# Kernel tuning notes

Hardware: AMD Instinct MI355X
Metric: run time of the kernel (lower is better)

## Reference

```python
import jax, jax.numpy as jnp
import numpy as np

B, T, D_MODEL, HEAD_DIM = 16, 4096, 512, 64


def setup_inputs() -> dict:
    key = jax.random.key(0)
    kx, kq, kk, kv = jax.random.split(key, 4)
    x = jax.random.normal(kx, (B, T, D_MODEL), dtype=jnp.float32)
    # torch nn.Linear weights, stored pre-transposed as [in, out] for x @ W
    s = 1.0 / np.sqrt(D_MODEL)
    Wq = jax.random.uniform(kq, (D_MODEL, HEAD_DIM), jnp.float32, -s, s)
    Wk = jax.random.uniform(kk, (D_MODEL, HEAD_DIM), jnp.float32, -s, s)
    Wv = jax.random.uniform(kv, (D_MODEL, HEAD_DIM), jnp.float32, -s, s)
    return {"x": x, "Wq": Wq, "Wk": Wk, "Wv": Wv}


def reference(x, Wq, Wk, Wv):
    # Single-head causal self-attention (dropout in eval mode = identity)
    q = x @ Wq  # [B, T, h]
    k = x @ Wk
    v = x @ Wv
    scale = 1.0 / np.sqrt(HEAD_DIM).astype(np.float32)
    scores = jnp.einsum("bth,bsh->bts", q, k) * scale  # [B, T, T]
    t = scores.shape[1]
    causal = jnp.tril(jnp.ones((t, t), dtype=bool))
    scores = jnp.where(causal, scores, -jnp.inf)
    weights = jax.nn.softmax(scores, axis=-1)
    return jnp.einsum("bts,bsh->bth", weights, v)  # [B, T, h]
```

## Files before the change

### kernel.cpp

```cpp
#include <hip/hip_runtime.h>
#include <hip/hip_bf16.h>
#include <math.h>


#define NB 16
#define NT 4096
#define DMODEL 512
#define HD 64
#define CEXP 0.18033688011112042f

typedef unsigned short u16;
typedef unsigned int u32;
typedef __attribute__((ext_vector_type(2))) unsigned int u32x2;
typedef __attribute__((ext_vector_type(8))) short bf16x8;
typedef __attribute__((ext_vector_type(4))) float f32x4;
typedef __attribute__((ext_vector_type(16))) float f32x16;

__device__ __forceinline__ u16 bfu(float x) {
  __hip_bfloat16 h = __float2bfloat16(x);
  return *(u16*)&h;
}

__device__ __forceinline__ u32 cvtpk(float lo, float hi) {
  u32 r;
  asm("v_cvt_pk_bf16_f32 %0, %1, %2" : "=v"(r) : "v"(lo), "v"(hi));
  return r;
}

__device__ __forceinline__ u32x2 lane_swap(u32 a, u32 b) {
  asm("v_permlane32_swap_b32 %0, %1" : "+v"(a), "+v"(b));
  u32x2 r; r[0] = a; r[1] = b; return r;
}

__device__ __forceinline__ void gload16(const void* g, void* l) {
  __builtin_amdgcn_global_load_lds(
      (const __attribute__((address_space(1))) void*)g,
      (__attribute__((address_space(3))) void*)l, 16, 0, 0);
}

#define MFMA32(a, b, c) __builtin_amdgcn_mfma_f32_16x16x32_bf16(a, b, c, 0, 0, 0)
#define WMFMA(a, b, c)  __builtin_amdgcn_mfma_f32_32x32x16_bf16(a, b, c, 0, 0, 0)
#define LD8(p) (*(const bf16x8*)(p))

__global__ void prep_wt(const float* __restrict__ Wq, const float* __restrict__ Wk,
                        const float* __restrict__ Wv, u16* __restrict__ Wt) {
  int k0 = blockIdx.x * 16;
  int t = threadIdx.x;
#pragma unroll
  for (int i = 0; i < 12; ++i) {
    int idx = t + i * 256;
    int n = idx % 192;
    int kk = idx / 192;
    const float* W = (n < 64) ? Wq : (n < 128) ? Wk : Wv;
    float w = W[(size_t)(k0 + kk) * 64 + (n & 63)];
    Wt[(size_t)n * 512 + k0 + kk] = bfu(w);
  }
}

__global__ __launch_bounds__(512) void proj_qkv(const float* __restrict__ x,
                                                const u16* __restrict__ Wt,
                                                u16* __restrict__ qo,
                                                u16* __restrict__ ko,
                                                u16* __restrict__ vo) {
  __shared__ u16 As[2][128][48];
  int t = threadIdx.x;
  int m0 = blockIdx.x * 128;
  int lane = t & 63, wid = t >> 6;
  int wr = wid >> 2, wc = wid & 3;
  int g = lane >> 4, li = lane & 15;
  f32x4 acc[4][3];
#pragma unroll
  for (int i = 0; i < 4; ++i)
#pragma unroll
    for (int j = 0; j < 3; ++j) acc[i][j] = (f32x4){0.f, 0.f, 0.f, 0.f};

  int row = t >> 2, quad = t & 3;
  const float* srcb = x + (size_t)(m0 + row) * DMODEL + quad * 8;

  float4 pa0[3], pa1[3];
#pragma unroll
  for (int s = 0; s < 3; ++s) {
    pa0[s] = *(const float4*)(srcb + s * 32);
    pa1[s] = *(const float4*)(srcb + s * 32 + 4);
  }

#pragma unroll
  for (int s = 0; s < 16; ++s) {
    float4 c0 = pa0[s % 3], c1 = pa1[s % 3];
    if (s + 3 < 16) {
      pa0[s % 3] = *(const float4*)(srcb + (s + 3) * 32);
      pa1[s % 3] = *(const float4*)(srcb + (s + 3) * 32 + 4);
    }
    union { u16 u[8]; bf16x8 v; } tmp;
    tmp.u[0] = bfu(c0.x); tmp.u[1] = bfu(c0.y);
    tmp.u[2] = bfu(c0.z); tmp.u[3] = bfu(c0.w);
    tmp.u[4] = bfu(c1.x); tmp.u[5] = bfu(c1.y);
    tmp.u[6] = bfu(c1.z); tmp.u[7] = bfu(c1.w);
    *(bf16x8*)&As[s & 1][row][quad * 8] = tmp.v;
    __syncthreads();

    int k0 = s * 32;
    bf16x8 a[4], bb[3];
#pragma unroll
    for (int mf = 0; mf < 4; ++mf)
      a[mf] = *(const bf16x8*)&As[s & 1][wr * 64 + mf * 16 + li][g * 8];
#pragma unroll
    for (int nf = 0; nf < 3; ++nf)
      bb[nf] = *(const bf16x8*)(Wt + (size_t)(wc * 48 + nf * 16 + li) * 512 + k0 + g * 8);
#pragma unroll
    for (int mf = 0; mf < 4; ++mf)
#pragma unroll
      for (int nf = 0; nf < 3; ++nf)
        acc[mf][nf] = MFMA32(a[mf], bb[nf], acc[mf][nf]);
  }

#pragma unroll
  for (int nf = 0; nf < 3; ++nf) {
    int n = wc * 48 + nf * 16 + li;
    if (n < 64) {
      int col = n;
#pragma unroll
      for (int mf = 0; mf < 4; ++mf)
#pragma unroll
        for (int r = 0; r < 4; ++r) {
          int m = m0 + wr * 64 + mf * 16 + 4 * g + r;
          qo[(size_t)m * HD + col] = bfu(acc[mf][nf][r] * CEXP);
        }
    } else if (n < 128) {
      int col = n & 63;
      int dt = col >> 4, hh = (col >> 3) & 1, jj = col & 7;
      size_t fo = (size_t)(dt * 2 + hh) * 256 + jj;
#pragma unroll
      for (int mf = 0; mf < 4; ++mf)
#pragma unroll
        for (int r = 0; r < 4; ++r) {
          int m = m0 + wr * 64 + mf * 16 + 4 * g + r;
          ko[(size_t)(m >> 5) * 2048 + fo + (m & 31) * 8] = bfu(acc[mf][nf][r]);
        }
    } else {
      int d = n - 128;
      int dh = d >> 5, l31d = d & 31;
#pragma unroll
      for (int mf = 0; mf < 4; ++mf) {
        int mbase = m0 + wr * 64 + mf * 16 + 4 * g;
        int kk2 = mbase & 31;
        int kt2 = kk2 >> 4, hh = (kk2 >> 3) & 1;
        size_t off = (size_t)(mbase >> 5) * 2048 +
                     (size_t)((dh * 2 + kt2) * 2 + hh) * 256 + l31d * 8 + (mbase & 7);
        ushort4 pk;
        pk.x = bfu(acc[mf][nf][0]);
        pk.y = bfu(acc[mf][nf][1]);
        pk.z = bfu(acc[mf][nf][2]);
        pk.w = bfu(acc[mf][nf][3]);
        *(ushort4*)(vo + off) = pk;
      }
    }
  }
}

__global__ __launch_bounds__(256, 2) void attn_fwd13(const u16* __restrict__ qg,
                                                     const u16* __restrict__ kg,
                                                     const u16* __restrict__ vg,
                                                     float* __restrict__ out) {
  __shared__ __align__(16) char smem[65536];
  u16* KV = (u16*)smem;
  float* MrgF = (float*)smem;

  int tid = threadIdx.x;
  int lane = tid & 63, w = tid >> 6;
  int l31 = lane & 31, h = lane >> 5;
  int qi = w >> 1, ki = w & 1;

  int f = blockIdx.x;
  int xcd = f & 7, i = f >> 3;
  int b = 2 * xcd + (i & 1);
  int bp = 63 - (i >> 1);

  const int limb = 2 * bp + 1;
  const int diagw = 2 * bp + qi;
  const int nr = (bp + 2) >> 1;
  const int q0w = bp * 64 + qi * 32;

  const u16* qb = qg + (size_t)b * NT * HD;
  const u16* kbs = kg + (size_t)b * NT * HD;
  const u16* vbs = vg + (size_t)b * NT * HD;
  float* ob = out + (size_t)b * NT * HD;

  bf16x8 qf[4];
#pragma unroll
  for (int dt = 0; dt < 4; ++dt)
    qf[dt] = LD8(qb + (size_t)(q0w + l31) * HD + dt * 16 + 8 * h);

  f32x16 oacc0, oacc1;
#pragma unroll
  for (int r = 0; r < 16; ++r) { oacc0[r] = 0.f; oacc1[r] = 0.f; }
  float lsum = 0.f;

  auto STAGE = [&](u16* lb, int tg) {
    const u16* gk = kbs + (size_t)tg * 2048 + lane * 8;
    const u16* gv = vbs + (size_t)tg * 2048 + lane * 8;
    u16* dk = lb + w * 4096 + lane * 8;
#pragma unroll
    for (int ii = 0; ii < 4; ++ii) {
      gload16(gk + ii * 512, dk + ii * 512);
      gload16(gv + ii * 512, dk + 2048 + ii * 512);
    }
  };

  auto COMPUTE = [&](const u16* kp0, const u16* vp0, bool maskdiag) {
    bf16x8 kf[4], vf[4];
#pragma unroll
    for (int dt = 0; dt < 4; ++dt)
      kf[dt] = LD8(kp0 + dt * 512 + h * 256 + l31 * 8);
#pragma unroll
    for (int dv = 0; dv < 4; ++dv)
      vf[dv] = LD8(vp0 + dv * 512 + h * 256 + l31 * 8);

    f32x16 sv;
#pragma unroll
    for (int r = 0; r < 16; ++r) sv[r] = 0.f;
    sv = WMFMA(kf[0], qf[0], sv);
    sv = WMFMA(kf[1], qf[1], sv);
    sv = WMFMA(kf[2], qf[2], sv);
    sv = WMFMA(kf[3], qf[3], sv);

    if (maskdiag) {
#pragma unroll
      for (int r = 0; r < 16; ++r) {
        int key = (r & 3) + 8 * (r >> 2) + 4 * h;
        if (key > l31) sv[r] = -1e30f;
      }
    }

    float p[16];
#pragma unroll
    for (int r = 0; r < 16; ++r) p[r] = __builtin_amdgcn_exp2f(sv[r]);
    lsum += (((p[0] + p[1]) + (p[2] + p[3])) + ((p[4] + p[5]) + (p[6] + p[7]))) +
            (((p[8] + p[9]) + (p[10] + p[11])) + ((p[12] + p[13]) + (p[14] + p[15])));
    u32 A0 = cvtpk(p[0], p[1]),   A1 = cvtpk(p[2], p[3]);
    u32 B0 = cvtpk(p[4], p[5]),   B1 = cvtpk(p[6], p[7]);
    u32 C0 = cvtpk(p[8], p[9]),   C1 = cvtpk(p[10], p[11]);
    u32 E0 = cvtpk(p[12], p[13]), E1 = cvtpk(p[14], p[15]);
    u32x2 s0 = lane_swap(A0, B0), s1 = lane_swap(A1, B1);
    u32x2 s2 = lane_swap(C0, E0), s3 = lane_swap(C1, E1);
    union { u32 d[4]; bf16x8 v; } f0u, f1u;
    f0u.d[0] = s0[0]; f0u.d[1] = s1[0]; f0u.d[2] = s0[1]; f0u.d[3] = s1[1];
    f1u.d[0] = s2[0]; f1u.d[1] = s3[0]; f1u.d[2] = s2[1]; f1u.d[3] = s3[1];

    oacc0 = WMFMA(vf[0], f0u.v, oacc0);
    oacc1 = WMFMA(vf[2], f0u.v, oacc1);
    oacc0 = WMFMA(vf[1], f1u.v, oacc0);
    oacc1 = WMFMA(vf[3], f1u.v, oacc1);
  };

  STAGE(KV, min(w, limb));

  int cur = 0;
  for (int jr = 0; jr < nr; ++jr) {
    if (jr + 1 < nr) {
      STAGE(KV + (cur ^ 1) * 16384, min(4 * (jr + 1) + w, limb));
      asm volatile("s_waitcnt vmcnt(8)" ::: "memory");
    } else {
      asm volatile("s_waitcnt vmcnt(0)" ::: "memory");
    }
    __builtin_amdgcn_sched_barrier(0);
    asm volatile("s_barrier" ::: "memory");

    const u16* kv0 = KV + cur * 16384;
    int j1 = 4 * jr + ki, j2 = 4 * jr + 2 + ki;
    __builtin_amdgcn_s_setprio(1);
    if (j1 <= diagw)
      COMPUTE(kv0 + ki * 4096, kv0 + ki * 4096 + 2048, j1 == diagw);
    if (j2 <= diagw)
      COMPUTE(kv0 + (2 + ki) * 4096, kv0 + (2 + ki) * 4096 + 2048, j2 == diagw);
    __builtin_amdgcn_s_setprio(0);

    asm volatile("s_barrier" ::: "memory");
    cur ^= 1;
  }

  lsum += __shfl_xor(lsum, 32);
  {
    float* mg = MrgF + ((size_t)w * 64 + lane) * 33;
#pragma unroll
    for (int r = 0; r < 16; ++r) { mg[r] = oacc0[r]; mg[16 + r] = oacc1[r]; }
    mg[32] = lsum;
  }
  __syncthreads();
#pragma unroll
  for (int s = 0; s < 4; ++s) {
    int ql = (lane >> 2) + 16 * (s & 1);
    int dq = ki * 8 + (lane & 3) + 4 * (s >> 1);
    const float* m0p = MrgF + ((size_t)(qi * 2) * 64) * 33;
    const float* m1p = MrgF + ((size_t)(qi * 2 + 1) * 64) * 33;
    float ls = m0p[(size_t)ql * 33 + 32] + m1p[(size_t)ql * 33 + 32];
    float inv = 1.0f / ls;
    f32x4 o4;
#pragma unroll
    for (int dd = 0; dd < 4; ++dd) {
      int d = dq * 4 + dd;
      int dh = d >> 5, rem = d & 31;
      int srch = (rem >> 2) & 1;
      int reg = dh * 16 + (rem & 3) + ((rem >> 3) << 2);
      size_t ro = (size_t)(ql + 32 * srch) * 33 + reg;
      o4[dd] = (m0p[ro] + m1p[ro]) * inv;
    }
    *(f32x4*)(ob + (size_t)(q0w + ql) * HD + dq * 4) = o4;
  }
}

extern "C" void kernel_launch(void* const* d_in, const int* in_sizes, int n_in,
                              void* d_out, int out_size, void* d_ws, size_t ws_size,
                              hipStream_t stream) {
  const float* x  = (const float*)d_in[0];
  const float* Wq = (const float*)d_in[1];
  const float* Wk = (const float*)d_in[2];
  const float* Wv = (const float*)d_in[3];
  float* out = (float*)d_out;

  u16* Wt  = (u16*)d_ws;
  u16* qws = (u16*)((char*)d_ws + 192 * 512 * 2);
  u16* kws = qws + (size_t)NB * NT * HD;
  u16* vws = kws + (size_t)NB * NT * HD;

  prep_wt<<<32, 256, 0, stream>>>(Wq, Wk, Wv, Wt);
  proj_qkv<<<(NB * NT) / 128, 512, 0, stream>>>(x, Wt, qws, kws, vws);
  attn_fwd13<<<1024, 256, 0, stream>>>(qws, kws, vws, out);
}
```

Measured before the change: 91.09 us.

## Load V straight to registers and halve LDS to allow three blocks per CU

```diff
diff --git a/kernel.cpp b/kernel.cpp
--- a/kernel.cpp
+++ b/kernel.cpp
@@ -158,11 +158,11 @@
   }
 }
 
-__global__ __launch_bounds__(256, 2) void attn_fwd13(const u16* __restrict__ qg,
+__global__ __launch_bounds__(256, 3) void attn_fwd14(const u16* __restrict__ qg,
                                                      const u16* __restrict__ kg,
                                                      const u16* __restrict__ vg,
                                                      float* __restrict__ out) {
-  __shared__ __align__(16) char smem[65536];
+  __shared__ __align__(16) char smem[32768];
   u16* KV = (u16*)smem;
   float* MrgF = (float*)smem;
 
@@ -196,25 +196,25 @@
   for (int r = 0; r < 16; ++r) { oacc0[r] = 0.f; oacc1[r] = 0.f; }
   float lsum = 0.f;
 
-  auto STAGE = [&](u16* lb, int tg) {
+  auto STAGEK = [&](u16* lb, int tg) {
     const u16* gk = kbs + (size_t)tg * 2048 + lane * 8;
-    const u16* gv = vbs + (size_t)tg * 2048 + lane * 8;
-    u16* dk = lb + w * 4096 + lane * 8;
-#pragma unroll
-    for (int ii = 0; ii < 4; ++ii) {
+    u16* dk = lb + w * 2048 + lane * 8;
+#pragma unroll
+    for (int ii = 0; ii < 4; ++ii)
       gload16(gk + ii * 512, dk + ii * 512);
-      gload16(gv + ii * 512, dk + 2048 + ii * 512);
-    }
   };
-
-  auto COMPUTE = [&](const u16* kp0, const u16* vp0, bool maskdiag) {
-    bf16x8 kf[4], vf[4];
+  auto LOADV = [&](bf16x8 (&vf)[4], int jj) {
+    const u16* vp = vbs + (size_t)jj * 2048 + h * 256 + l31 * 8;
+#pragma unroll
+    for (int dv = 0; dv < 4; ++dv)
+      vf[dv] = LD8(vp + dv * 512);
+  };
+
+  auto COMPUTE = [&](const u16* kp0, const bf16x8 (&vf)[4], bool maskdiag) {
+    bf16x8 kf[4];
 #pragma unroll
     for (int dt = 0; dt < 4; ++dt)
       kf[dt] = LD8(kp0 + dt * 512 + h * 256 + l31 * 8);
-#pragma unroll
-    for (int dv = 0; dv < 4; ++dv)
-      vf[dv] = LD8(vp0 + dv * 512 + h * 256 + l31 * 8);
 
     f32x16 sv;
 #pragma unroll
@@ -253,26 +253,27 @@
     oacc1 = WMFMA(vf[3], f1u.v, oacc1);
   };
 
-  STAGE(KV, min(w, limb));
+  STAGEK(KV, min(w, limb));
 
   int cur = 0;
   for (int jr = 0; jr < nr; ++jr) {
+    int j1 = 4 * jr + ki, j2 = 4 * jr + 2 + ki;
+    bf16x8 vf1[4], vf2[4];
+    LOADV(vf1, min(j1, 127));
+    LOADV(vf2, min(j2, 127));
     if (jr + 1 < nr) {
-      STAGE(KV + (cur ^ 1) * 16384, min(4 * (jr + 1) + w, limb));
+      STAGEK(KV + (cur ^ 1) * 8192, min(4 * (jr + 1) + w, limb));
+      asm volatile("s_waitcnt vmcnt(12)" ::: "memory");
+    } else {
       asm volatile("s_waitcnt vmcnt(8)" ::: "memory");
-    } else {
-      asm volatile("s_waitcnt vmcnt(0)" ::: "memory");
     }
     __builtin_amdgcn_sched_barrier(0);
     asm volatile("s_barrier" ::: "memory");
 
-    const u16* kv0 = KV + cur * 16384;
-    int j1 = 4 * jr + ki, j2 = 4 * jr + 2 + ki;
+    const u16* kv0 = KV + cur * 8192;
     __builtin_amdgcn_s_setprio(1);
-    if (j1 <= diagw)
-      COMPUTE(kv0 + ki * 4096, kv0 + ki * 4096 + 2048, j1 == diagw);
-    if (j2 <= diagw)
-      COMPUTE(kv0 + (2 + ki) * 4096, kv0 + (2 + ki) * 4096 + 2048, j2 == diagw);
+    if (j1 <= diagw) COMPUTE(kv0 + ki * 2048, vf1, j1 == diagw);
+    if (j2 <= diagw) COMPUTE(kv0 + (2 + ki) * 2048, vf2, j2 == diagw);
     __builtin_amdgcn_s_setprio(0);
 
     asm volatile("s_barrier" ::: "memory");
@@ -280,32 +281,36 @@
   }
 
   lsum += __shfl_xor(lsum, 32);
-  {
-    float* mg = MrgF + ((size_t)w * 64 + lane) * 33;
-#pragma unroll
-    for (int r = 0; r < 16; ++r) { mg[r] = oacc0[r]; mg[16 + r] = oacc1[r]; }
-    mg[32] = lsum;
-  }
-  __syncthreads();
-#pragma unroll
-  for (int s = 0; s < 4; ++s) {
-    int ql = (lane >> 2) + 16 * (s & 1);
-    int dq = ki * 8 + (lane & 3) + 4 * (s >> 1);
-    const float* m0p = MrgF + ((size_t)(qi * 2) * 64) * 33;
-    const float* m1p = MrgF + ((size_t)(qi * 2 + 1) * 64) * 33;
-    float ls = m0p[(size_t)ql * 33 + 32] + m1p[(size_t)ql * 33 + 32];
-    float inv = 1.0f / ls;
-    f32x4 o4;
-#pragma unroll
-    for (int dd = 0; dd < 4; ++dd) {
-      int d = dq * 4 + dd;
-      int dh = d >> 5, rem = d & 31;
-      int srch = (rem >> 2) & 1;
-      int reg = dh * 16 + (rem & 3) + ((rem >> 3) << 2);
-      size_t ro = (size_t)(ql + 32 * srch) * 33 + reg;
-      o4[dd] = (m0p[ro] + m1p[ro]) * inv;
-    }
-    *(f32x4*)(ob + (size_t)(q0w + ql) * HD + dq * 4) = o4;
+#pragma unroll
+  for (int s = 0; s < 2; ++s) {
+    if (s) __syncthreads();
+    {
+      float* mg = MrgF + ((size_t)w * 64 + lane) * 17;
+      const f32x16& oS = s ? oacc1 : oacc0;
+#pragma unroll
+      for (int r = 0; r < 16; ++r) mg[r] = oS[r];
+      mg[16] = lsum;
+    }
+    __syncthreads();
+    const float* m0p = MrgF + ((size_t)(qi * 2) * 64) * 17;
+    const float* m1p = MrgF + ((size_t)(qi * 2 + 1) * 64) * 17;
+#pragma unroll
+    for (int t2 = 0; t2 < 2; ++t2) {
+      int ql = (lane >> 2) + 16 * t2;
+      float ls = m0p[(size_t)ql * 17 + 16] + m1p[(size_t)ql * 17 + 16];
+      float inv = 1.0f / ls;
+      f32x4 o4;
+#pragma unroll
+      for (int dd = 0; dd < 4; ++dd) {
+        int rem = ki * 16 + (lane & 3) * 4 + dd;
+        int srch = (rem >> 2) & 1;
+        int reg = (rem & 3) + ((rem >> 3) << 2);
+        size_t ro = (size_t)(ql + 32 * srch) * 17 + reg;
+        o4[dd] = (m0p[ro] + m1p[ro]) * inv;
+      }
+      int d0 = s * 32 + ki * 16 + (lane & 3) * 4;
+      *(f32x4*)(ob + (size_t)(q0w + ql) * HD + d0) = o4;
+    }
   }
 }
 
@@ -325,5 +330,5 @@
 
   prep_wt<<<32, 256, 0, stream>>>(Wq, Wk, Wv, Wt);
   proj_qkv<<<(NB * NT) / 128, 512, 0, stream>>>(x, Wt, qws, kws, vws);
-  attn_fwd13<<<1024, 256, 0, stream>>>(qws, kws, vws, out);
-}
+  attn_fwd14<<<1024, 256, 0, stream>>>(qws, kws, vws, out);
+}
```

Result: slower. 93.68 us, median of 2 (+2.8%).
